# Kernel tuning notes

Hardware: AMD Instinct MI355X
Metric: run time of the kernel (lower is better)

The kernel has to match this reference:

```python
import jax, jax.numpy as jnp
import numpy as np

NB_HEAD = 8
SIZE_PER_HEAD = 64
MAX_LEN = 1024
D_IN = 512
BATCH = 8
NEG_BIG = 1e12  # matches the torch module's mask * 1000000000000.0


def setup_inputs() -> dict:
    key = jax.random.key(0)
    ks = jax.random.split(key, 6)
    return {
        "Q_seq": jax.random.normal(ks[0], (BATCH, MAX_LEN, D_IN), dtype=jnp.float32),
        "K_seq": jax.random.normal(ks[1], (BATCH, MAX_LEN, D_IN), dtype=jnp.float32),
        "V_seq": jax.random.normal(ks[2], (BATCH, MAX_LEN, D_IN), dtype=jnp.float32),
        "WQ": jax.random.normal(ks[3], (D_IN, NB_HEAD * SIZE_PER_HEAD), dtype=jnp.float32),
        "WK": jax.random.normal(ks[4], (D_IN, NB_HEAD * SIZE_PER_HEAD), dtype=jnp.float32),
        "WV": jax.random.normal(ks[5], (D_IN, NB_HEAD * SIZE_PER_HEAD), dtype=jnp.float32),
    }


def reference(Q_seq, K_seq, V_seq, WQ, WK, WV):
    B, L, _ = Q_seq.shape
    H, D = NB_HEAD, SIZE_PER_HEAD
    # QKV projections -> [B, H, L, D]
    q = (Q_seq @ WQ).reshape(B, L, H, D).transpose(0, 2, 1, 3)
    k = (K_seq @ WK).reshape(B, L, H, D).transpose(0, 2, 1, 3)
    v = (V_seq @ WV).reshape(B, L, H, D).transpose(0, 2, 1, 3)
    # scaled dot-product scores [B, H, Lq, Lk]
    scores = jnp.einsum("bhqd,bhkd->bhqk", q, k) / jnp.sqrt(jnp.float32(D))
    # causal mask: the torch Mask() subtracts 1e12 where key_idx > query_idx
    causal = jnp.triu(jnp.ones((L, L), dtype=scores.dtype), k=1)  # 1 where k > q
    scores = scores - causal[None, None, :, :] * NEG_BIG
    attn = jax.nn.softmax(scores, axis=-1)
    out = jnp.einsum("bhqk,bhkd->bhqd", attn, v)  # [B, H, L, D]
    return out.transpose(0, 2, 1, 3).reshape(B, L, H * D)
```

## Files before the change

kernel.cpp:

```cpp
#include <hip/hip_runtime.h>
#include <cstddef>

#define LEN    1024
#define DIN    512
#define NHEAD  8
#define HDIM   64
#define BATCH  8

typedef __attribute__((ext_vector_type(8))) short  short8;
typedef __attribute__((ext_vector_type(4))) float  f32x4;

#define MFMA16(a, b, c) __builtin_amdgcn_mfma_f32_16x16x32_bf16((a), (b), (c), 0, 0, 0)

__device__ __forceinline__ unsigned short bf_hi(float x) {
    unsigned u = __float_as_uint(x);
    return (unsigned short)((u + 0x7fffu + ((u >> 16) & 1u)) >> 16);
}
__device__ __forceinline__ void bf_split(float x, unsigned short& h, unsigned short& l) {
    unsigned u  = __float_as_uint(x);
    unsigned hu = (u + 0x7fffu + ((u >> 16) & 1u)) >> 16;
    h = (unsigned short)hu;
    l = bf_hi(x - __uint_as_float(hu << 16));
}
__device__ __forceinline__ void unpack4(uint4 u, ushort4& h, ushort4& l) {
    h = make_ushort4((unsigned short)(u.x >> 16), (unsigned short)(u.y >> 16),
                     (unsigned short)(u.z >> 16), (unsigned short)(u.w >> 16));
    l = make_ushort4((unsigned short)(u.x & 0xffff), (unsigned short)(u.y & 0xffff),
                     (unsigned short)(u.z & 0xffff), (unsigned short)(u.w & 0xffff));
}

template<int CTRL>
__device__ __forceinline__ float dpp_mov(float x) {
    return __int_as_float(__builtin_amdgcn_update_dpp(
        0, __float_as_int(x), CTRL, 0xF, 0xF, true));
}
__device__ __forceinline__ float red16_max(float x) {
    x = fmaxf(x, dpp_mov<0xB1>(x));
    x = fmaxf(x, dpp_mov<0x4E>(x));
    x = fmaxf(x, dpp_mov<0x141>(x));
    x = fmaxf(x, dpp_mov<0x140>(x));
    return x;
}
__device__ __forceinline__ float red16_sum(float x) {
    x += dpp_mov<0xB1>(x);
    x += dpp_mov<0x4E>(x);
    x += dpp_mov<0x141>(x);
    x += dpp_mov<0x140>(x);
    return x;
}

__global__ __launch_bounds__(256)
void wprep(const float* __restrict__ WQ, const float* __restrict__ WK,
           const float* __restrict__ WV, unsigned short* __restrict__ wt)
{
    __shared__ float T[64][68];
    const int z = blockIdx.z;
    const float* W = (z == 0) ? WQ : (z == 1) ? WK : WV;
    unsigned short* Wth = wt + (size_t)z * 524288;
    unsigned short* Wtl = Wth + 262144;
    const int k0 = blockIdx.x * 64, n0 = blockIdx.y * 64;
    const int t = threadIdx.x;
    #pragma unroll
    for (int e = 0; e < 4; ++e) {
        int f = e * 256 + t, r = f >> 4, c4 = (f & 15) << 2;
        *(float4*)&T[r][c4] = *(const float4*)&W[(size_t)(k0 + r) * 512 + n0 + c4];
    }
    __syncthreads();
    #pragma unroll
    for (int e = 0; e < 4; ++e) {
        int f = e * 256 + t, nr = f >> 4, kc4 = (f & 15) << 2;
        ushort4 h, l;
        bf_split(T[kc4 + 0][nr], h.x, l.x);
        bf_split(T[kc4 + 1][nr], h.y, l.y);
        bf_split(T[kc4 + 2][nr], h.z, l.z);
        bf_split(T[kc4 + 3][nr], h.w, l.w);
        *(ushort4*)&Wth[(size_t)(n0 + nr) * 512 + k0 + kc4] = h;
        *(ushort4*)&Wtl[(size_t)(n0 + nr) * 512 + k0 + kc4] = l;
    }
}

#define PSTR 40

__global__ __launch_bounds__(256)
void proj_mfma(const float* __restrict__ Qin, const float* __restrict__ Kin,
               const float* __restrict__ Vin, const unsigned short* __restrict__ wt,
               unsigned int* __restrict__ qhl, unsigned int* __restrict__ khl,
               unsigned short* __restrict__ vh)
{
    __shared__ unsigned short Ah[128 * PSTR], Al[128 * PSTR],
                              Bh[128 * PSTR], Bl[128 * PSTR];
    const int z = blockIdx.z;
    const float* X = (z == 0) ? Qin : (z == 1) ? Kin : Vin;
    const unsigned short* Wth = wt + (size_t)z * 524288;
    const unsigned short* Wtl = Wth + 262144;

    const int t = threadIdx.x, lane = t & 63, w = t >> 6;
    const int wm = w & 1, wn = w >> 1;
    const int m0 = blockIdx.x * 128, n0 = blockIdx.y * 128;
    const int lm = lane & 15, lq = lane >> 4;
    const int ar = t >> 1, ak = (t & 1) * 16;

    const float* Xp = X + (size_t)(m0 + ar) * 512 + ak;
    const unsigned short* Bph = Wth + (size_t)(n0 + ar) * 512 + ak;
    const unsigned short* Bpl = Wtl + (size_t)(n0 + ar) * 512 + ak;

    f32x4 acc[4][4];
    #pragma unroll
    for (int i = 0; i < 4; ++i)
        #pragma unroll
        for (int j = 0; j < 4; ++j) acc[i][j] = 0.f;

    float4 av[4];
    uint4 b0, b1, b2, b3;
    #pragma unroll
    for (int e = 0; e < 4; ++e) av[e] = *(const float4*)(Xp + e * 4);
    b0 = *(const uint4*)(Bph);
    b1 = *(const uint4*)(Bph + 8);
    b2 = *(const uint4*)(Bpl);
    b3 = *(const uint4*)(Bpl + 8);

    for (int k0 = 0; k0 < 512; k0 += 32) {
        __syncthreads();
        #pragma unroll
        for (int e = 0; e < 4; ++e) {
            ushort4 h, l;
            bf_split(av[e].x, h.x, l.x);
            bf_split(av[e].y, h.y, l.y);
            bf_split(av[e].z, h.z, l.z);
            bf_split(av[e].w, h.w, l.w);
            *(ushort4*)&Ah[ar * PSTR + ak + e * 4] = h;
            *(ushort4*)&Al[ar * PSTR + ak + e * 4] = l;
        }
        *(uint4*)&Bh[ar * PSTR + ak]     = b0;
        *(uint4*)&Bh[ar * PSTR + ak + 8] = b1;
        *(uint4*)&Bl[ar * PSTR + ak]     = b2;
        *(uint4*)&Bl[ar * PSTR + ak + 8] = b3;
        __syncthreads();

        if (k0 + 32 < 512) {
            #pragma unroll
            for (int e = 0; e < 4; ++e) av[e] = *(const float4*)(Xp + k0 + 32 + e * 4);
            b0 = *(const uint4*)(Bph + k0 + 32);
            b1 = *(const uint4*)(Bph + k0 + 40);
            b2 = *(const uint4*)(Bpl + k0 + 32);
            b3 = *(const uint4*)(Bpl + k0 + 40);
        }

        short8 a_h[4], a_l[4];
        #pragma unroll
        for (int mi = 0; mi < 4; ++mi) {
            int off = (wm * 64 + mi * 16 + lm) * PSTR + lq * 8;
            a_h[mi] = *(const short8*)&Ah[off];
            a_l[mi] = *(const short8*)&Al[off];
        }
        #pragma unroll
        for (int ni = 0; ni < 4; ++ni) {
            int off = (wn * 64 + ni * 16 + lm) * PSTR + lq * 8;
            short8 b_h = *(const short8*)&Bh[off];
            short8 b_l = *(const short8*)&Bl[off];
            #pragma unroll
            for (int mi = 0; mi < 4; ++mi) {
                acc[mi][ni] = MFMA16(a_l[mi], b_h, acc[mi][ni]);
                acc[mi][ni] = MFMA16(a_h[mi], b_l, acc[mi][ni]);
                acc[mi][ni] = MFMA16(a_h[mi], b_h, acc[mi][ni]);
            }
        }
    }

    if (z < 2) {
        unsigned int* o = (z == 0) ? qhl : khl;
        const float sc = (z == 0) ? 0.18033688011112042f : 1.0f;
        #pragma unroll
        for (int mi = 0; mi < 4; ++mi)
            #pragma unroll
            for (int ni = 0; ni < 4; ++ni) {
                int n_abs = n0 + wn * 64 + ni * 16 + lm;
                int hd = n_abs >> 6, d = n_abs & 63;
                #pragma unroll
                for (int r = 0; r < 4; ++r) {
                    int m_abs = m0 + wm * 64 + mi * 16 + lq * 4 + r;
                    int b = m_abs >> 10, li = m_abs & 1023;
                    unsigned short hv, lv;
                    bf_split(acc[mi][ni][r] * sc, hv, lv);
                    o[(((size_t)b * NHEAD + hd) * LEN + li) * HDIM + d] =
                        ((unsigned)hv << 16) | lv;
                }
            }
    } else {
        #pragma unroll
        for (int mi = 0; mi < 4; ++mi) {
            int m_base = m0 + wm * 64 + mi * 16 + lq * 4;
            int b = m_base >> 10, l0 = m_base & 1023;
            #pragma unroll
            for (int ni = 0; ni < 4; ++ni) {
                int n_abs = n0 + wn * 64 + ni * 16 + lm;
                int hd = n_abs >> 6, d = n_abs & 63;
                ushort4 hv = make_ushort4(bf_hi(acc[mi][ni][0]), bf_hi(acc[mi][ni][1]),
                                          bf_hi(acc[mi][ni][2]), bf_hi(acc[mi][ni][3]));
                *(ushort4*)&vh[(((size_t)b * NHEAD + hd) * HDIM + d) * LEN + l0] = hv;
            }
        }
    }
}

__global__ __launch_bounds__(256)
void attn_mfma(const unsigned int* __restrict__ qhl, const unsigned int* __restrict__ khl,
               const unsigned short* __restrict__ vth, float* __restrict__ out)
{
    __shared__ unsigned short sm[23040];
    unsigned short* Kh  = sm;
    unsigned short* Kl  = sm + 4608;
    unsigned short* Vt  = sm + 9216;
    unsigned short* Pb  = sm + 13824;
    unsigned short* Qsh = sm;
    unsigned short* Qsl = sm + 9216;

    const int t = threadIdx.x, lane = t & 63, w = t >> 6;
    const int lm = lane & 15, lq = lane >> 4;
    const int bx = blockIdx.x;
    const int qt = 7 - (bx >> 6);
    const int bh = bx & 63;
    const size_t base = (size_t)bh * LEN * HDIM;
    const unsigned int*   qb = qhl + base;
    const unsigned int*   kb = khl + base;
    const unsigned short* vb = vth + base;
    const int Q0  = qt * 128;
    const int Q0w = Q0 + w * 32;

    #pragma unroll
    for (int e = 0; e < 8; ++e) {
        int f = e * 256 + t, r = f >> 4, c4 = (f & 15) << 2;
        uint4 u = *(const uint4*)&qb[(size_t)(Q0 + r) * 64 + c4];
        ushort4 h, l;
        unpack4(u, h, l);
        *(ushort4*)&Qsh[r * 72 + c4] = h;
        *(ushort4*)&Qsl[r * 72 + c4] = l;
    }
    __syncthreads();
    short8 qfh[2][2], qfl[2][2];
    #pragma unroll
    for (int mi = 0; mi < 2; ++mi)
        #pragma unroll
        for (int ks = 0; ks < 2; ++ks) {
            int off = (w * 32 + mi * 16 + lm) * 72 + ks * 32 + lq * 8;
            qfh[mi][ks] = *(const short8*)&Qsh[off];
            qfl[mi][ks] = *(const short8*)&Qsl[off];
        }

    float m_i[2][4], l_i[2][4];
    f32x4 oacc[2][4];
    #pragma unroll
    for (int mi = 0; mi < 2; ++mi)
        #pragma unroll
        for (int r = 0; r < 4; ++r) { m_i[mi][r] = -1e30f; l_i[mi][r] = 0.f; }
    #pragma unroll
    for (int mi = 0; mi < 2; ++mi)
        #pragma unroll
        for (int nd = 0; nd < 4; ++nd) oacc[mi][nd] = 0.f;

    const int kr_ = t >> 4, kc4 = (t & 15) << 2;
    const int vd_ = t >> 3, vs8 = (t & 7) << 3;

    uint4 kreg[4], vreg[2];
    #pragma unroll
    for (int e = 0; e < 4; ++e)
        kreg[e] = *(const uint4*)&kb[(size_t)(e * 16 + kr_) * 64 + kc4];
    #pragma unroll
    for (int e = 0; e < 2; ++e)
        vreg[e] = *(const uint4*)&vb[(size_t)(e * 32 + vd_) * LEN + vs8];

    const int jend = 2 * qt + 1;
    for (int jb = 0; jb <= jend; ++jb) {
        __syncthreads();
        #pragma unroll
        for (int e = 0; e < 4; ++e) {
            int r = e * 16 + kr_;
            ushort4 h, l;
            unpack4(kreg[e], h, l);
            *(ushort4*)&Kh[r * 72 + kc4] = h;
            *(ushort4*)&Kl[r * 72 + kc4] = l;
        }
        #pragma unroll
        for (int e = 0; e < 2; ++e)
            *(uint4*)&Vt[(e * 32 + vd_) * 72 + vs8] = vreg[e];
        __syncthreads();

        if (jb < jend) {
            #pragma unroll
            for (int e = 0; e < 4; ++e)
                kreg[e] = *(const uint4*)&kb[(size_t)((jb + 1) * 64 + e * 16 + kr_) * 64 + kc4];
            #pragma unroll
            for (int e = 0; e < 2; ++e)
                vreg[e] = *(const uint4*)&vb[(size_t)(e * 32 + vd_) * LEN + (jb + 1) * 64 + vs8];
        }

        const bool active = (jb * 64 <= Q0w + 31);
        if (active) {
            f32x4 sf[2][4];
            #pragma unroll
            for (int mi = 0; mi < 2; ++mi)
                #pragma unroll
                for (int ni = 0; ni < 4; ++ni) sf[mi][ni] = 0.f;
            #pragma unroll
            for (int ks = 0; ks < 2; ++ks)
                #pragma unroll
                for (int ni = 0; ni < 4; ++ni) {
                    int off = (ni * 16 + lm) * 72 + ks * 32 + lq * 8;
                    short8 b_h = *(const short8*)&Kh[off];
                    short8 b_l = *(const short8*)&Kl[off];
                    #pragma unroll
                    for (int mi = 0; mi < 2; ++mi) {
                        sf[mi][ni] = MFMA16(qfl[mi][ks], b_h, sf[mi][ni]);
                        sf[mi][ni] = MFMA16(qfh[mi][ks], b_l, sf[mi][ni]);
                        sf[mi][ni] = MFMA16(qfh[mi][ks], b_h, sf[mi][ni]);
                    }
                }
            if (jb * 64 + 63 > Q0w) {
                #pragma unroll
                for (int mi = 0; mi < 2; ++mi)
                    #pragma unroll
                    for (int ni = 0; ni < 4; ++ni) {
                        int key = jb * 64 + ni * 16 + lm;
                        #pragma unroll
                        for (int r = 0; r < 4; ++r) {
                            int qi = Q0w + mi * 16 + lq * 4 + r;
                            if (key > qi) sf[mi][ni][r] = -1e30f;
                        }
                    }
            }
            #pragma unroll
            for (int mi = 0; mi < 2; ++mi)
                #pragma unroll
                for (int r = 0; r < 4; ++r) {
                    float mv = fmaxf(fmaxf(sf[mi][0][r], sf[mi][1][r]),
                                     fmaxf(sf[mi][2][r], sf[mi][3][r]));
                    mv = red16_max(mv);
                    float mo = m_i[mi][r];
                    float mn = fmaxf(mo, mv);
                    float al = __builtin_amdgcn_exp2f(mo - mn);
                    m_i[mi][r] = mn;
                    float rs = 0.f;
                    int prow = (w * 32 + mi * 16 + lq * 4 + r) * 72 + lm;
                    #pragma unroll
                    for (int ni = 0; ni < 4; ++ni) {
                        float p = __builtin_amdgcn_exp2f(sf[mi][ni][r] - mn);
                        rs += p;
                        Pb[prow + ni * 16] = bf_hi(p);
                    }
                    rs = red16_sum(rs);
                    l_i[mi][r] = l_i[mi][r] * al + rs;
                    #pragma unroll
                    for (int nd = 0; nd < 4; ++nd) oacc[mi][nd][r] *= al;
                }
            short8 pf[2][2];
            #pragma unroll
            for (int mi = 0; mi < 2; ++mi)
                #pragma unroll
                for (int ks = 0; ks < 2; ++ks)
                    pf[mi][ks] = *(const short8*)&Pb[(w * 32 + mi * 16 + lm) * 72 + ks * 32 + lq * 8];
            #pragma unroll
            for (int ks = 0; ks < 2; ++ks)
                #pragma unroll
                for (int nd = 0; nd < 4; ++nd) {
                    short8 vf = *(const short8*)&Vt[(nd * 16 + lm) * 72 + ks * 32 + lq * 8];
                    #pragma unroll
                    for (int mi = 0; mi < 2; ++mi)
                        oacc[mi][nd] = MFMA16(pf[mi][ks], vf, oacc[mi][nd]);
                }
        }
    }

    const int b = bh >> 3, hd = bh & 7;
    #pragma unroll
    for (int mi = 0; mi < 2; ++mi)
        #pragma unroll
        for (int r = 0; r < 4; ++r) {
            int qrow = Q0w + mi * 16 + lq * 4 + r;
            float inv = 1.0f / l_i[mi][r];
            #pragma unroll
            for (int nd = 0; nd < 4; ++nd) {
                int d = nd * 16 + lm;
                out[((size_t)b * LEN + qrow) * (NHEAD * HDIM) + hd * 64 + d] =
                    oacc[mi][nd][r] * inv;
            }
        }
}

extern "C" void kernel_launch(void* const* d_in, const int* in_sizes, int n_in,
                              void* d_out, int out_size, void* d_ws, size_t ws_size,
                              hipStream_t stream)
{
    const float* Qin = (const float*)d_in[0];
    const float* Kin = (const float*)d_in[1];
    const float* Vin = (const float*)d_in[2];
    const float* WQ  = (const float*)d_in[3];
    const float* WK  = (const float*)d_in[4];
    const float* WV  = (const float*)d_in[5];

    const size_t per = (size_t)BATCH * NHEAD * LEN * HDIM;
    unsigned int*   qhl = (unsigned int*)d_ws;
    unsigned int*   khl = qhl + per;
    unsigned short* vh  = (unsigned short*)(khl + per);
    unsigned short* wt  = vh + per;

    wprep    <<<dim3(8, 8, 3),  256, 0, stream>>>(WQ, WK, WV, wt);
    proj_mfma<<<dim3(64, 4, 3), 256, 0, stream>>>(Qin, Kin, Vin, wt, qhl, khl, vh);
    attn_mfma<<<dim3(512),      256, 0, stream>>>(qhl, khl, vh, (float*)d_out);
}
```

Measured before the change: 202.1 us.

## Use single-bf16 V projection, perm-based packing, and alias P buffer in attention LDS

The V projection now does one bf16 MFMA per tile instead of the three-term hi/lo split, and skips the low-part loads and stores. This is justified because V is rounded to bf16 on output anyway. The A hi parts are now built by truncation and packed with v_perm, and K hi/lo unpacking in attention uses perm on wider contiguous loads. The attention P buffer now aliases the K tile, with an extra barrier between scores and softmax, to shrink LDS and allow higher occupancy. The trade-offs are slightly lower V accuracy and one extra sync per key block.

```diff
diff --git a/kernel.cpp b/kernel.cpp
--- a/kernel.cpp
+++ b/kernel.cpp
@@ -11,6 +11,8 @@
 typedef __attribute__((ext_vector_type(4))) float  f32x4;
 
 #define MFMA16(a, b, c) __builtin_amdgcn_mfma_f32_16x16x32_bf16((a), (b), (c), 0, 0, 0)
+#define PERM_HI 0x07060302u
+#define PERM_LO 0x05040100u
 
 __device__ __forceinline__ unsigned short bf_hi(float x) {
     unsigned u = __float_as_uint(x);
@@ -27,6 +29,16 @@
                      (unsigned short)(u.z >> 16), (unsigned short)(u.w >> 16));
     l = make_ushort4((unsigned short)(u.x & 0xffff), (unsigned short)(u.y & 0xffff),
                      (unsigned short)(u.z & 0xffff), (unsigned short)(u.w & 0xffff));
+}
+__device__ __forceinline__ void unpack8(uint4 a, uint4 b, uint4& h, uint4& l) {
+    h = make_uint4(__builtin_amdgcn_perm(a.y, a.x, PERM_HI),
+                   __builtin_amdgcn_perm(a.w, a.z, PERM_HI),
+                   __builtin_amdgcn_perm(b.y, b.x, PERM_HI),
+                   __builtin_amdgcn_perm(b.w, b.z, PERM_HI));
+    l = make_uint4(__builtin_amdgcn_perm(a.y, a.x, PERM_LO),
+                   __builtin_amdgcn_perm(a.w, a.z, PERM_LO),
+                   __builtin_amdgcn_perm(b.y, b.x, PERM_LO),
+                   __builtin_amdgcn_perm(b.w, b.z, PERM_LO));
 }
 
 template<int CTRL>
@@ -90,6 +102,7 @@
     __shared__ unsigned short Ah[128 * PSTR], Al[128 * PSTR],
                               Bh[128 * PSTR], Bl[128 * PSTR];
     const int z = blockIdx.z;
+    const bool full = (z < 2);
     const float* X = (z == 0) ? Qin : (z == 1) ? Kin : Vin;
     const unsigned short* Wth = wt + (size_t)z * 524288;
     const unsigned short* Wtl = Wth + 262144;
@@ -111,39 +124,59 @@
         for (int j = 0; j < 4; ++j) acc[i][j] = 0.f;
 
     float4 av[4];
-    uint4 b0, b1, b2, b3;
+    uint4 bh0, bh1, bl0, bl1;
     #pragma unroll
     for (int e = 0; e < 4; ++e) av[e] = *(const float4*)(Xp + e * 4);
-    b0 = *(const uint4*)(Bph);
-    b1 = *(const uint4*)(Bph + 8);
-    b2 = *(const uint4*)(Bpl);
-    b3 = *(const uint4*)(Bpl + 8);
+    bh0 = *(const uint4*)(Bph);
+    bh1 = *(const uint4*)(Bph + 8);
+    if (full) { bl0 = *(const uint4*)(Bpl); bl1 = *(const uint4*)(Bpl + 8); }
 
     for (int k0 = 0; k0 < 512; k0 += 32) {
         __syncthreads();
-        #pragma unroll
-        for (int e = 0; e < 4; ++e) {
-            ushort4 h, l;
-            bf_split(av[e].x, h.x, l.x);
-            bf_split(av[e].y, h.y, l.y);
-            bf_split(av[e].z, h.z, l.z);
-            bf_split(av[e].w, h.w, l.w);
-            *(ushort4*)&Ah[ar * PSTR + ak + e * 4] = h;
-            *(ushort4*)&Al[ar * PSTR + ak + e * 4] = l;
-        }
-        *(uint4*)&Bh[ar * PSTR + ak]     = b0;
-        *(uint4*)&Bh[ar * PSTR + ak + 8] = b1;
-        *(uint4*)&Bl[ar * PSTR + ak]     = b2;
-        *(uint4*)&Bl[ar * PSTR + ak + 8] = b3;
+        {
+            const float* ff = (const float*)&av[0];
+            uint hw[16];
+            #pragma unroll
+            for (int i = 0; i < 16; ++i) hw[i] = __float_as_uint(ff[i]) & 0xffff0000u;
+            uint4 ahv  = make_uint4(__builtin_amdgcn_perm(hw[1],  hw[0],  PERM_HI),
+                                    __builtin_amdgcn_perm(hw[3],  hw[2],  PERM_HI),
+                                    __builtin_amdgcn_perm(hw[5],  hw[4],  PERM_HI),
+                                    __builtin_amdgcn_perm(hw[7],  hw[6],  PERM_HI));
+            uint4 ahv2 = make_uint4(__builtin_amdgcn_perm(hw[9],  hw[8],  PERM_HI),
+                                    __builtin_amdgcn_perm(hw[11], hw[10], PERM_HI),
+                                    __builtin_amdgcn_perm(hw[13], hw[12], PERM_HI),
+                                    __builtin_amdgcn_perm(hw[15], hw[14], PERM_HI));
+            *(uint4*)&Ah[ar * PSTR + ak]     = ahv;
+            *(uint4*)&Ah[ar * PSTR + ak + 8] = ahv2;
+            if (full) {
+                uint lo[8];
+                #pragma unroll
+                for (int i = 0; i < 8; ++i) {
+                    float r0 = ff[2*i]   - __uint_as_float(hw[2*i]);
+                    float r1 = ff[2*i+1] - __uint_as_float(hw[2*i+1]);
+                    lo[i] = ((uint)bf_hi(r1) << 16) | bf_hi(r0);
+                }
+                *(uint4*)&Al[ar * PSTR + ak]     = make_uint4(lo[0], lo[1], lo[2], lo[3]);
+                *(uint4*)&Al[ar * PSTR + ak + 8] = make_uint4(lo[4], lo[5], lo[6], lo[7]);
+            }
+        }
+        *(uint4*)&Bh[ar * PSTR + ak]     = bh0;
+        *(uint4*)&Bh[ar * PSTR + ak + 8] = bh1;
+        if (full) {
+            *(uint4*)&Bl[ar * PSTR + ak]     = bl0;
+            *(uint4*)&Bl[ar * PSTR + ak + 8] = bl1;
+        }
         __syncthreads();
 
         if (k0 + 32 < 512) {
             #pragma unroll
             for (int e = 0; e < 4; ++e) av[e] = *(const float4*)(Xp + k0 + 32 + e * 4);
-            b0 = *(const uint4*)(Bph + k0 + 32);
-            b1 = *(const uint4*)(Bph + k0 + 40);
-            b2 = *(const uint4*)(Bpl + k0 + 32);
-            b3 = *(const uint4*)(Bpl + k0 + 40);
+            bh0 = *(const uint4*)(Bph + k0 + 32);
+            bh1 = *(const uint4*)(Bph + k0 + 40);
+            if (full) {
+                bl0 = *(const uint4*)(Bpl + k0 + 32);
+                bl1 = *(const uint4*)(Bpl + k0 + 40);
+            }
         }
 
         short8 a_h[4], a_l[4];
@@ -151,18 +184,24 @@
         for (int mi = 0; mi < 4; ++mi) {
             int off = (wm * 64 + mi * 16 + lm) * PSTR + lq * 8;
             a_h[mi] = *(const short8*)&Ah[off];
-            a_l[mi] = *(const short8*)&Al[off];
+            if (full) a_l[mi] = *(const short8*)&Al[off];
         }
         #pragma unroll
         for (int ni = 0; ni < 4; ++ni) {
             int off = (wn * 64 + ni * 16 + lm) * PSTR + lq * 8;
             short8 b_h = *(const short8*)&Bh[off];
-            short8 b_l = *(const short8*)&Bl[off];
-            #pragma unroll
-            for (int mi = 0; mi < 4; ++mi) {
-                acc[mi][ni] = MFMA16(a_l[mi], b_h, acc[mi][ni]);
-                acc[mi][ni] = MFMA16(a_h[mi], b_l, acc[mi][ni]);
-                acc[mi][ni] = MFMA16(a_h[mi], b_h, acc[mi][ni]);
+            if (full) {
+                short8 b_l = *(const short8*)&Bl[off];
+                #pragma unroll
+                for (int mi = 0; mi < 4; ++mi) {
+                    acc[mi][ni] = MFMA16(a_l[mi], b_h, acc[mi][ni]);
+                    acc[mi][ni] = MFMA16(a_h[mi], b_l, acc[mi][ni]);
+                    acc[mi][ni] = MFMA16(a_h[mi], b_h, acc[mi][ni]);
+                }
+            } else {
+                #pragma unroll
+                for (int mi = 0; mi < 4; ++mi)
+                    acc[mi][ni] = MFMA16(a_h[mi], b_h, acc[mi][ni]);
             }
         }
     }
@@ -207,11 +246,11 @@
 void attn_mfma(const unsigned int* __restrict__ qhl, const unsigned int* __restrict__ khl,
                const unsigned short* __restrict__ vth, float* __restrict__ out)
 {
-    __shared__ unsigned short sm[23040];
+    __shared__ unsigned short sm[18432];
     unsigned short* Kh  = sm;
     unsigned short* Kl  = sm + 4608;
+    unsigned short* Pb  = sm;
     unsigned short* Vt  = sm + 9216;
-    unsigned short* Pb  = sm + 13824;
     unsigned short* Qsh = sm;
     unsigned short* Qsl = sm + 9216;
 
@@ -258,13 +297,13 @@
         #pragma unroll
         for (int nd = 0; nd < 4; ++nd) oacc[mi][nd] = 0.f;
 
-    const int kr_ = t >> 4, kc4 = (t & 15) << 2;
+    const int kr = t >> 2, kq = t & 3;
     const int vd_ = t >> 3, vs8 = (t & 7) << 3;
 
     uint4 kreg[4], vreg[2];
     #pragma unroll
     for (int e = 0; e < 4; ++e)
-        kreg[e] = *(const uint4*)&kb[(size_t)(e * 16 + kr_) * 64 + kc4];
+        kreg[e] = *(const uint4*)&kb[(size_t)kr * 64 + kq * 16 + e * 4];
     #pragma unroll
     for (int e = 0; e < 2; ++e)
         vreg[e] = *(const uint4*)&vb[(size_t)(e * 32 + vd_) * LEN + vs8];
@@ -272,31 +311,32 @@
     const int jend = 2 * qt + 1;
     for (int jb = 0; jb <= jend; ++jb) {
         __syncthreads();
-        #pragma unroll
-        for (int e = 0; e < 4; ++e) {
-            int r = e * 16 + kr_;
-            ushort4 h, l;
-            unpack4(kreg[e], h, l);
-            *(ushort4*)&Kh[r * 72 + kc4] = h;
-            *(ushort4*)&Kl[r * 72 + kc4] = l;
-        }
-        #pragma unroll
-        for (int e = 0; e < 2; ++e)
-            *(uint4*)&Vt[(e * 32 + vd_) * 72 + vs8] = vreg[e];
+        {
+            uint4 h0, l0, h1, l1;
+            unpack8(kreg[0], kreg[1], h0, l0);
+            unpack8(kreg[2], kreg[3], h1, l1);
+            int ko = kr * 72 + kq * 16;
+            *(uint4*)&Kh[ko]     = h0;
+            *(uint4*)&Kh[ko + 8] = h1;
+            *(uint4*)&Kl[ko]     = l0;
+            *(uint4*)&Kl[ko + 8] = l1;
+            *(uint4*)&Vt[(vd_)      * 72 + vs8] = vreg[0];
+            *(uint4*)&Vt[(vd_ + 32) * 72 + vs8] = vreg[1];
+        }
         __syncthreads();
 
         if (jb < jend) {
             #pragma unroll
             for (int e = 0; e < 4; ++e)
-                kreg[e] = *(const uint4*)&kb[(size_t)((jb + 1) * 64 + e * 16 + kr_) * 64 + kc4];
+                kreg[e] = *(const uint4*)&kb[(size_t)((jb + 1) * 64 + kr) * 64 + kq * 16 + e * 4];
             #pragma unroll
             for (int e = 0; e < 2; ++e)
                 vreg[e] = *(const uint4*)&vb[(size_t)(e * 32 + vd_) * LEN + (jb + 1) * 64 + vs8];
         }
 
         const bool active = (jb * 64 <= Q0w + 31);
+        f32x4 sf[2][4];
         if (active) {
-            f32x4 sf[2][4];
             #pragma unroll
             for (int mi = 0; mi < 2; ++mi)
                 #pragma unroll
@@ -328,6 +368,10 @@
                         }
                     }
             }
+        }
+        __syncthreads();
+
+        if (active) {
             #pragma unroll
             for (int mi = 0; mi < 2; ++mi)
                 #pragma unroll
```

Result: faster. 189.3 us (-6.3%).
